# Kernel tuning notes

Hardware: AMD Instinct MI355X
Metric: run time of the kernel (lower is better)

Reference implementation:

```python
import jax, jax.numpy as jnp
import numpy as np

EPS = 1e-9


def setup_inputs() -> dict:
    key = jax.random.key(0)
    k1, k2, k3, k4 = jax.random.split(key, 4)
    B, N = 8192, 256
    T, Q = 4096, 64
    reprs = jax.random.normal(k1, (B, N), dtype=jnp.float32)
    memory = jax.random.normal(k2, (T, Q, N), dtype=jnp.float32)
    # memory bank rows are kept unit-norm by the module's renormalization
    memory = memory / (jnp.linalg.norm(memory, axis=-1, keepdims=True) + EPS)
    alpha = jax.random.uniform(k3, (Q, 1), dtype=jnp.float32)
    track_idxs = jax.random.randint(k4, (B,), 0, T, dtype=jnp.int64)
    return {"reprs": reprs, "memory": memory, "alpha": alpha, "track_idxs": track_idxs}


def reference(reprs, memory, alpha, track_idxs):
    # Vectorized equivalent of MemoryBank.update (init != 'zeros' branch):
    # per track t present in track_idxs, per slot q:
    #   b* = argmin_{b: track_idxs[b]==t} <memory[t,q], reprs[b]>   (first occurrence)
    #   m  = alpha[q] * memory[t,q] + (1-alpha[q]) * reprs[b*]
    #   memory[t,q] = m / (||m|| + eps)
    B, N = reprs.shape
    T, Q, _ = memory.shape
    tid = track_idxs.astype(jnp.int32)

    # similarity of each detection against its own track's Q slots: [B, Q]
    sim = jnp.einsum('bqn,bn->bq', memory[tid], reprs)

    # segment-min over detections of each track -> [T, Q]
    min_val = jnp.full((T, Q), jnp.inf, dtype=sim.dtype).at[tid].min(sim)
    # first detection index achieving the min (matches torch argmin tie-break)
    b_idx = jnp.arange(B, dtype=jnp.int32)[:, None]                 # [B, 1]
    cand = jnp.where(sim == min_val[tid], b_idx, B)                 # [B, Q]
    chosen = jnp.full((T, Q), B, dtype=jnp.int32).at[tid].min(cand)  # [T, Q]

    present = chosen[:, 0] < B                                       # [T]
    sel = reprs[jnp.minimum(chosen, B - 1)]                          # [T, Q, N]

    upd = memory * alpha + sel * (1.0 - alpha)                       # alpha: [Q,1]
    upd = upd / (jnp.linalg.norm(upd, axis=-1, keepdims=True) + EPS)
    return jnp.where(present[:, None, None], upd, memory)
```

## Files before the change

kernel.cpp:

```cpp
#include <hip/hip_runtime.h>
#include <stdint.h>

#define B_DET 8192
#define N_DIM 256
#define T_TRK 4096
#define Q_SLOT 64
#define MAXD   64
#define EPSF   1e-9f

typedef unsigned long long ull;
typedef float nfloat4 __attribute__((ext_vector_type(4)));

__device__ __forceinline__ uint32_t f32_key(float f) {
    uint32_t u = __float_as_uint(f);
    return (u & 0x80000000u) ? ~u : (u | 0x80000000u);
}
__device__ __forceinline__ float key_inv(uint32_t k) {
    uint32_t u = (k & 0x80000000u) ? (k ^ 0x80000000u) : ~k;
    return __uint_as_float(u);
}

__device__ __forceinline__ void nt_store_f4(float* p, float4 v) {
    nfloat4 nv; nv.x = v.x; nv.y = v.y; nv.z = v.z; nv.w = v.w;
    __builtin_nontemporal_store(nv, reinterpret_cast<nfloat4*>(p));
}

__global__ __launch_bounds__(256)
void build_lists(const int* __restrict__ track_idxs,
                 int* __restrict__ cnt, int* __restrict__ list) {
    const int b = blockIdx.x * 256 + threadIdx.x;
    const int t = track_idxs[b];
    const int slot = atomicAdd(&cnt[t], 1);
    if (slot < MAXD) list[t * MAXD + slot] = b;
}

__global__ __launch_bounds__(256)
void row_norms(const float* __restrict__ reprs, float* __restrict__ norm2) {
    const int row  = blockIdx.x * 4 + (threadIdx.x >> 6);
    const int lane = threadIdx.x & 63;
    const float4 v = reinterpret_cast<const float4*>(reprs + (size_t)row * N_DIM)[lane];
    float ss = v.x * v.x + v.y * v.y + v.z * v.z + v.w * v.w;
    #pragma unroll
    for (int o = 32; o >= 1; o >>= 1) ss += __shfl_xor(ss, o, 64);
    if (lane == 0) norm2[row] = ss;
}

__global__ __launch_bounds__(256)
void fused_update(const float* __restrict__ reprs,
                  const float* __restrict__ memory,
                  const float* __restrict__ alpha,
                  const int* __restrict__ cnt,
                  const int* __restrict__ list,
                  const float* __restrict__ norm2,
                  float* __restrict__ out) {
    const int bid  = blockIdx.x;
    const int swz  = (bid & 7) * (8192 >> 3) + (bid >> 3);
    const int t    = swz >> 1;
    const int wave = threadIdx.x >> 6;
    const int lane = threadIdx.x & 63;
    const int g    = lane >> 4;
    const int cidx = lane & 15;
    const int qbase = (swz & 1) * 32 + wave * 8;
    const size_t tbase = (size_t)t * Q_SLOT * N_DIM;

    int D = cnt[t];
    if (D == 0) {
        const size_t rbase = tbase + (size_t)qbase * N_DIM;
        float4 mm[8];
        #pragma unroll
        for (int s = 0; s < 8; ++s)
            mm[s] = reinterpret_cast<const float4*>(memory + rbase + (size_t)s * N_DIM)[lane];
        #pragma unroll
        for (int s = 0; s < 8; ++s)
            nt_store_f4(out + rbase + (size_t)s * N_DIM + lane * 4, mm[s]);
        return;
    }
    if (D > MAXD) D = MAXD;

    float4 m[2][4];
    #pragma unroll
    for (int i = 0; i < 2; ++i) {
        const float* rp = memory + tbase + (size_t)(qbase + i * 4 + g) * N_DIM;
        #pragma unroll
        for (int c = 0; c < 4; ++c)
            m[i][c] = reinterpret_cast<const float4*>(rp)[cidx + c * 16];
    }

    ull best[2] = { ~0ULL, ~0ULL };

    int b_cur = list[t * MAXD];
    float4 rc[4];
    {
        const float* rp = reprs + (size_t)b_cur * N_DIM;
        #pragma unroll
        for (int cc = 0; cc < 4; ++cc)
            rc[cc] = reinterpret_cast<const float4*>(rp)[cidx + cc * 16];
    }

    for (int d = 0; d < D; ++d) {
        int b_nxt = 0;
        float4 rn[4];
        if (d + 1 < D) {
            b_nxt = list[t * MAXD + d + 1];
            const float* rp = reprs + (size_t)b_nxt * N_DIM;
            #pragma unroll
            for (int cc = 0; cc < 4; ++cc)
                rn[cc] = reinterpret_cast<const float4*>(rp)[cidx + cc * 16];
        }

        float p0 = 0.0f, p1 = 0.0f;
        #pragma unroll
        for (int cc = 0; cc < 4; ++cc) {
            p0 += m[0][cc].x * rc[cc].x + m[0][cc].y * rc[cc].y
                + m[0][cc].z * rc[cc].z + m[0][cc].w * rc[cc].w;
            p1 += m[1][cc].x * rc[cc].x + m[1][cc].y * rc[cc].y
                + m[1][cc].z * rc[cc].z + m[1][cc].w * rc[cc].w;
        }
        #pragma unroll
        for (int o = 8; o >= 1; o >>= 1) {
            p0 += __shfl_xor(p0, o, 64);
            p1 += __shfl_xor(p1, o, 64);
        }

        const uint32_t bd = ((uint32_t)b_cur << 6) | (uint32_t)d;
        const ull k0 = ((ull)f32_key(p0) << 32) | bd;
        const ull k1 = ((ull)f32_key(p1) << 32) | bd;
        if (k0 < best[0]) best[0] = k0;
        if (k1 < best[1]) best[1] = k1;

        b_cur = b_nxt;
        #pragma unroll
        for (int cc = 0; cc < 4; ++cc) rc[cc] = rn[cc];
    }

    #pragma unroll
    for (int i = 0; i < 2; ++i) {
        const int q = qbase + i * 4 + g;
        const int   bsel = (int)(((uint32_t)best[i]) >> 6);
        const float dot  = key_inv((uint32_t)(best[i] >> 32));
        const float a    = alpha[q];
        const float na   = 1.0f - a;

        const float* rp = reprs + (size_t)bsel * N_DIM;
        const float nrm2 = a * a + na * na * norm2[bsel] + 2.0f * a * na * dot;
        const float sc = 1.0f / (sqrtf(nrm2) + EPSF);

        float* op = out + tbase + (size_t)q * N_DIM;
        #pragma unroll
        for (int cc = 0; cc < 4; ++cc) {
            const float4 r = reinterpret_cast<const float4*>(rp)[cidx + cc * 16];
            float4 u;
            u.x = (a * m[i][cc].x + na * r.x) * sc;
            u.y = (a * m[i][cc].y + na * r.y) * sc;
            u.z = (a * m[i][cc].z + na * r.z) * sc;
            u.w = (a * m[i][cc].w + na * r.w) * sc;
            nt_store_f4(op + (cidx + cc * 16) * 4, u);
        }
    }
}

extern "C" void kernel_launch(void* const* d_in, const int* in_sizes, int n_in,
                              void* d_out, int out_size, void* d_ws, size_t ws_size,
                              hipStream_t stream) {
    const float* reprs      = (const float*)d_in[0];
    const float* memory     = (const float*)d_in[1];
    const float* alpha      = (const float*)d_in[2];
    const int*   track_idxs = (const int*)d_in[3];
    float*       out        = (float*)d_out;

    int*   cnt   = (int*)d_ws;
    int*   list  = (int*)((char*)d_ws + T_TRK * sizeof(int));
    float* norm2 = (float*)((char*)d_ws + T_TRK * sizeof(int)
                            + (size_t)T_TRK * MAXD * sizeof(int));

    (void)hipMemsetAsync(cnt, 0, T_TRK * sizeof(int), stream);
    build_lists<<<B_DET / 256, 256, 0, stream>>>(track_idxs, cnt, list);
    row_norms<<<B_DET / 4, 256, 0, stream>>>(reprs, norm2);
    fused_update<<<T_TRK * 2, 256, 0, stream>>>(reprs, memory, alpha, cnt, list, norm2, out);
}
```

Before: 96.83 us.

## Merge list-build and norm kernels; process one track per block with 16 slots per wave

```diff
diff --git a/kernel.cpp b/kernel.cpp
--- a/kernel.cpp
+++ b/kernel.cpp
@@ -26,23 +26,25 @@
 }
 
 __global__ __launch_bounds__(256)
-void build_lists(const int* __restrict__ track_idxs,
-                 int* __restrict__ cnt, int* __restrict__ list) {
-    const int b = blockIdx.x * 256 + threadIdx.x;
-    const int t = track_idxs[b];
-    const int slot = atomicAdd(&cnt[t], 1);
-    if (slot < MAXD) list[t * MAXD + slot] = b;
-}
+void prep(const float* __restrict__ reprs, const int* __restrict__ track_idxs,
+          int* __restrict__ cnt, int* __restrict__ list,
+          float* __restrict__ norm2) {
+    const int wave = threadIdx.x >> 6;
+    const int lane = threadIdx.x & 63;
+    const int row  = blockIdx.x * 4 + wave;
 
-__global__ __launch_bounds__(256)
-void row_norms(const float* __restrict__ reprs, float* __restrict__ norm2) {
-    const int row  = blockIdx.x * 4 + (threadIdx.x >> 6);
-    const int lane = threadIdx.x & 63;
     const float4 v = reinterpret_cast<const float4*>(reprs + (size_t)row * N_DIM)[lane];
     float ss = v.x * v.x + v.y * v.y + v.z * v.z + v.w * v.w;
     #pragma unroll
     for (int o = 32; o >= 1; o >>= 1) ss += __shfl_xor(ss, o, 64);
     if (lane == 0) norm2[row] = ss;
+
+    if (threadIdx.x < 4) {
+        const int b = blockIdx.x * 4 + threadIdx.x;
+        const int t = track_idxs[b];
+        const int slot = atomicAdd(&cnt[t], 1);
+        if (slot < MAXD) list[t * MAXD + slot] = b;
+    }
 }
 
 __global__ __launch_bounds__(256)
@@ -54,39 +56,38 @@
                   const float* __restrict__ norm2,
                   float* __restrict__ out) {
     const int bid  = blockIdx.x;
-    const int swz  = (bid & 7) * (8192 >> 3) + (bid >> 3);
-    const int t    = swz >> 1;
+    const int t    = (bid & 7) * (T_TRK >> 3) + (bid >> 3);
     const int wave = threadIdx.x >> 6;
     const int lane = threadIdx.x & 63;
     const int g    = lane >> 4;
     const int cidx = lane & 15;
-    const int qbase = (swz & 1) * 32 + wave * 8;
+    const int qb   = wave * 16;
     const size_t tbase = (size_t)t * Q_SLOT * N_DIM;
 
     int D = cnt[t];
     if (D == 0) {
-        const size_t rbase = tbase + (size_t)qbase * N_DIM;
-        float4 mm[8];
+        const size_t rbase = tbase + (size_t)qb * N_DIM;
+        float4 mm[16];
         #pragma unroll
-        for (int s = 0; s < 8; ++s)
+        for (int s = 0; s < 16; ++s)
             mm[s] = reinterpret_cast<const float4*>(memory + rbase + (size_t)s * N_DIM)[lane];
         #pragma unroll
-        for (int s = 0; s < 8; ++s)
+        for (int s = 0; s < 16; ++s)
             nt_store_f4(out + rbase + (size_t)s * N_DIM + lane * 4, mm[s]);
         return;
     }
     if (D > MAXD) D = MAXD;
 
-    float4 m[2][4];
+    float4 m[4][4];
     #pragma unroll
-    for (int i = 0; i < 2; ++i) {
-        const float* rp = memory + tbase + (size_t)(qbase + i * 4 + g) * N_DIM;
+    for (int u = 0; u < 4; ++u) {
+        const float* rp = memory + tbase + (size_t)(qb + u * 4 + g) * N_DIM;
         #pragma unroll
         for (int c = 0; c < 4; ++c)
-            m[i][c] = reinterpret_cast<const float4*>(rp)[cidx + c * 16];
+            m[u][c] = reinterpret_cast<const float4*>(rp)[cidx + c * 16];
     }
 
-    ull best[2] = { ~0ULL, ~0ULL };
+    ull best[4] = { ~0ULL, ~0ULL, ~0ULL, ~0ULL };
 
     int b_cur = list[t * MAXD];
     float4 rc[4];
@@ -108,25 +109,27 @@
                 rn[cc] = reinterpret_cast<const float4*>(rp)[cidx + cc * 16];
         }
 
-        float p0 = 0.0f, p1 = 0.0f;
+        float p[4] = { 0.0f, 0.0f, 0.0f, 0.0f };
         #pragma unroll
         for (int cc = 0; cc < 4; ++cc) {
-            p0 += m[0][cc].x * rc[cc].x + m[0][cc].y * rc[cc].y
-                + m[0][cc].z * rc[cc].z + m[0][cc].w * rc[cc].w;
-            p1 += m[1][cc].x * rc[cc].x + m[1][cc].y * rc[cc].y
-                + m[1][cc].z * rc[cc].z + m[1][cc].w * rc[cc].w;
+            #pragma unroll
+            for (int u = 0; u < 4; ++u)
+                p[u] += m[u][cc].x * rc[cc].x + m[u][cc].y * rc[cc].y
+                      + m[u][cc].z * rc[cc].z + m[u][cc].w * rc[cc].w;
         }
         #pragma unroll
         for (int o = 8; o >= 1; o >>= 1) {
-            p0 += __shfl_xor(p0, o, 64);
-            p1 += __shfl_xor(p1, o, 64);
+            #pragma unroll
+            for (int u = 0; u < 4; ++u)
+                p[u] += __shfl_xor(p[u], o, 64);
         }
 
         const uint32_t bd = ((uint32_t)b_cur << 6) | (uint32_t)d;
-        const ull k0 = ((ull)f32_key(p0) << 32) | bd;
-        const ull k1 = ((ull)f32_key(p1) << 32) | bd;
-        if (k0 < best[0]) best[0] = k0;
-        if (k1 < best[1]) best[1] = k1;
+        #pragma unroll
+        for (int u = 0; u < 4; ++u) {
+            const ull k = ((ull)f32_key(p[u]) << 32) | bd;
+            if (k < best[u]) best[u] = k;
+        }
 
         b_cur = b_nxt;
         #pragma unroll
@@ -134,10 +137,10 @@
     }
 
     #pragma unroll
-    for (int i = 0; i < 2; ++i) {
-        const int q = qbase + i * 4 + g;
-        const int   bsel = (int)(((uint32_t)best[i]) >> 6);
-        const float dot  = key_inv((uint32_t)(best[i] >> 32));
+    for (int u = 0; u < 4; ++u) {
+        const int q = qb + u * 4 + g;
+        const int   bsel = (int)(((uint32_t)best[u]) >> 6);
+        const float dot  = key_inv((uint32_t)(best[u] >> 32));
         const float a    = alpha[q];
         const float na   = 1.0f - a;
 
@@ -149,12 +152,12 @@
         #pragma unroll
         for (int cc = 0; cc < 4; ++cc) {
             const float4 r = reinterpret_cast<const float4*>(rp)[cidx + cc * 16];
-            float4 u;
-            u.x = (a * m[i][cc].x + na * r.x) * sc;
-            u.y = (a * m[i][cc].y + na * r.y) * sc;
-            u.z = (a * m[i][cc].z + na * r.z) * sc;
-            u.w = (a * m[i][cc].w + na * r.w) * sc;
-            nt_store_f4(op + (cidx + cc * 16) * 4, u);
+            float4 w;
+            w.x = (a * m[u][cc].x + na * r.x) * sc;
+            w.y = (a * m[u][cc].y + na * r.y) * sc;
+            w.z = (a * m[u][cc].z + na * r.z) * sc;
+            w.w = (a * m[u][cc].w + na * r.w) * sc;
+            nt_store_f4(op + (cidx + cc * 16) * 4, w);
         }
     }
 }
@@ -174,7 +177,6 @@
                             + (size_t)T_TRK * MAXD * sizeof(int));
 
     (void)hipMemsetAsync(cnt, 0, T_TRK * sizeof(int), stream);
-    build_lists<<<B_DET / 256, 256, 0, stream>>>(track_idxs, cnt, list);
-    row_norms<<<B_DET / 4, 256, 0, stream>>>(reprs, norm2);
-    fused_update<<<T_TRK * 2, 256, 0, stream>>>(reprs, memory, alpha, cnt, list, norm2, out);
+    prep<<<B_DET / 4, 256, 0, stream>>>(reprs, track_idxs, cnt, list, norm2);
+    fused_update<<<T_TRK, 256, 0, stream>>>(reprs, memory, alpha, cnt, list, norm2, out);
 }
```

Result: no change. 97.25 us (+0.4%).
